# Kernel tuning notes

Measured on AMD Instinct MI355X. Metric: run time of the kernel, lower is better.

The kernel has to match this reference:

```python
import jax, jax.numpy as jnp
import numpy as np

NEG_SLOPE = 0.2  # PyG GATConv default negative_slope


def gat_conv(x, src, dst, W, a_src, a_dst, b, concat):
    """One GATConv layer (PyG semantics, self-loops already included in src/dst).

    x: [N, F_in]; src, dst: [E] int; W: [F_in, H*C]; a_src, a_dst: [H, C]; b: bias.
    """
    N = x.shape[0]
    H, C = a_src.shape
    h = (x @ W).reshape(N, H, C)                      # projected node features
    alpha_src = jnp.sum(h * a_src, axis=-1)           # [N, H]
    alpha_dst = jnp.sum(h * a_dst, axis=-1)           # [N, H]
    logits = jax.nn.leaky_relu(alpha_src[src] + alpha_dst[dst], NEG_SLOPE)  # [E, H]
    # softmax over incoming edges of each destination node (numerically stable)
    m = jax.ops.segment_max(logits, dst, num_segments=N)                    # [N, H]
    p = jnp.exp(logits - m[dst])
    denom = jax.ops.segment_sum(p, dst, num_segments=N)                     # [N, H]
    alpha = p / denom[dst]                                                  # [E, H]
    # attention-weighted scatter-add aggregation
    out = jax.ops.segment_sum(alpha[:, :, None] * h[src], dst, num_segments=N)  # [N, H, C]
    out = out.reshape(N, H * C) if concat else out.mean(axis=1)
    return out + b


def setup_inputs() -> dict:
    key = jax.random.key(0)
    ks = jax.random.split(key, 10)
    N, E = 50000, 800000
    nfeats, hidden, nclasses, in_head, out_head = 256, 32, 40, 8, 1
    s = 0.05
    return {
        "x": jax.random.normal(ks[0], (N, nfeats), dtype=jnp.float32),
        "edge_index": jax.random.randint(ks[1], (2, E), 0, N, dtype=jnp.int32),
        "w1": jax.random.normal(ks[2], (nfeats, in_head * hidden), dtype=jnp.float32) * s,
        "a_src1": jax.random.normal(ks[3], (in_head, hidden), dtype=jnp.float32) * s,
        "a_dst1": jax.random.normal(ks[4], (in_head, hidden), dtype=jnp.float32) * s,
        "b1": jnp.zeros((in_head * hidden,), dtype=jnp.float32),
        "w2": jax.random.normal(ks[5], (in_head * hidden, out_head * nclasses), dtype=jnp.float32) * s,
        "a_src2": jax.random.normal(ks[6], (out_head, nclasses), dtype=jnp.float32) * s,
        "a_dst2": jax.random.normal(ks[7], (out_head, nclasses), dtype=jnp.float32) * s,
        "b2": jnp.zeros((nclasses,), dtype=jnp.float32),
    }


def reference(x, edge_index, w1, a_src1, a_dst1, b1, w2, a_src2, a_dst2, b2):
    N = x.shape[0]
    loops = jnp.arange(N, dtype=edge_index.dtype)
    src = jnp.concatenate([edge_index[0], loops])  # PyG add_self_loops=True
    dst = jnp.concatenate([edge_index[1], loops])
    h = gat_conv(x, src, dst, w1, a_src1, a_dst1, b1, concat=True)
    h = jax.nn.elu(h)
    out = gat_conv(h, src, dst, w2, a_src2, a_dst2, b2, concat=False)
    return out
```

## Files before the change

### kernel.cpp

```cpp
#include <hip/hip_runtime.h>
#include <cstdint>
#include <cstddef>

constexpr int Nn   = 50000;
constexpr int Ee   = 800000;
constexpr int ETot = Ee + Nn;
constexpr int H1   = 8;
constexpr int C1h  = 32;
constexpr int HC1  = 256;
constexpr int C2   = 40;
constexpr int S2   = 64;
constexpr float SLOPE = 0.2f;
constexpr int NB_SCAN = (Nn + 255) / 256;

typedef __attribute__((ext_vector_type(8))) short bf16x8;
typedef __attribute__((ext_vector_type(4))) float f32x4;

__device__ __forceinline__ ushort f2bf(float f) {
    uint u = __float_as_uint(f);
    u += 0x7fffu + ((u >> 16) & 1u);
    return (ushort)(u >> 16);
}
__device__ __forceinline__ float bf2f(ushort b) {
    return __uint_as_float(((uint)b) << 16);
}

__device__ __forceinline__ void gload16(const void* g, void* lds) {
    typedef const __attribute__((address_space(1))) unsigned int GU;
    typedef __attribute__((address_space(3))) unsigned int LU;
    __builtin_amdgcn_global_load_lds((GU*)g, (LU*)lds, 16, 0, 0);
}

__global__ void k_prep(const float* __restrict__ x, ushort* __restrict__ xhi,
                       ushort* __restrict__ xlo, const float* __restrict__ w1,
                       ushort* __restrict__ WT2, const float* __restrict__ w2,
                       ushort* __restrict__ WT2b, const int* __restrict__ dstA,
                       int* __restrict__ counts) {
    int t = blockIdx.x * blockDim.x + threadIdx.x;
    constexpr int n4 = Nn * HC1 / 4;
    if (t < n4) {
        float4 v = *(const float4*)(x + (size_t)t * 4);
        ushort4 h, l;
        h.x = f2bf(v.x); l.x = f2bf(v.x - bf2f(h.x));
        h.y = f2bf(v.y); l.y = f2bf(v.y - bf2f(h.y));
        h.z = f2bf(v.z); l.z = f2bf(v.z - bf2f(h.z));
        h.w = f2bf(v.w); l.w = f2bf(v.w - bf2f(h.w));
        *(ushort4*)(xhi + (size_t)t * 4) = h;
        *(ushort4*)(xlo + (size_t)t * 4) = l;
    }
    if (t < ETot) {
        int d = (t < Ee) ? dstA[t] : t - Ee;
        atomicAdd(&counts[d], 1);
    }
    if (t < 256 * 256) {
        int k = t >> 8, col = t & 255;
        float w = w1[(size_t)k * 256 + col];
        ushort h = f2bf(w), l = f2bf(w - bf2f(h));
        int kb = k >> 3, kr = k & 7;
        WT2[((size_t)(kb)      * 256 + col) * 8 + kr] = h;
        WT2[((size_t)(kb + 32) * 256 + col) * 8 + kr] = h;
        WT2[((size_t)(kb + 64) * 256 + col) * 8 + kr] = l;
    }
    if (t < 256 * 48) {
        int k = t / 48, col = t % 48;
        float w = (col < C2) ? w2[(size_t)k * C2 + col] : 0.f;
        ushort h = f2bf(w), l = f2bf(w - bf2f(h));
        int kb = k >> 3, kr = k & 7;
        WT2b[((size_t)(kb)      * 48 + col) * 8 + kr] = h;
        WT2b[((size_t)(kb + 32) * 48 + col) * 8 + kr] = h;
        WT2b[((size_t)(kb + 64) * 48 + col) * 8 + kr] = l;
    }
}

__global__ __launch_bounds__(256) void k_scan_block(const int* __restrict__ counts,
                                                    int* __restrict__ exsc,
                                                    int* __restrict__ bsum) {
    __shared__ int sm[256];
    int i = blockIdx.x * 256 + threadIdx.x;
    int v = (i < Nn) ? counts[i] : 0;
    sm[threadIdx.x] = v;
    __syncthreads();
#pragma unroll
    for (int off = 1; off < 256; off <<= 1) {
        int t = (threadIdx.x >= off) ? sm[threadIdx.x - off] : 0;
        __syncthreads();
        sm[threadIdx.x] += t;
        __syncthreads();
    }
    if (i < Nn) exsc[i] = sm[threadIdx.x] - v;
    if (threadIdx.x == 255) bsum[blockIdx.x] = sm[255];
}

__global__ __launch_bounds__(256) void k_scan_top(const int* __restrict__ bsum,
                                                  int* __restrict__ boff) {
    __shared__ int sm[256];
    int t = threadIdx.x;
    int v = (t < NB_SCAN) ? bsum[t] : 0;
    sm[t] = v;
    __syncthreads();
#pragma unroll
    for (int off = 1; off < 256; off <<= 1) {
        int x = (t >= off) ? sm[t - off] : 0;
        __syncthreads();
        sm[t] += x;
        __syncthreads();
    }
    if (t < NB_SCAN) boff[t] = sm[t] - v;
}

__global__ void k_finalize_off(const int* __restrict__ exsc, const int* __restrict__ boff,
                               int* __restrict__ row_off, int* __restrict__ cursor) {
    int i = blockIdx.x * blockDim.x + threadIdx.x;
    if (i < Nn) {
        int r = exsc[i] + boff[i >> 8];
        row_off[i] = r;
        cursor[i] = r;
    }
    if (i == 0) row_off[Nn] = ETot;
}

__global__ void k_scatter(const int* __restrict__ srcA, const int* __restrict__ dstA,
                          int* __restrict__ cursor, int* __restrict__ csr_src) {
    int e = blockIdx.x * blockDim.x + threadIdx.x;
    if (e >= ETot) return;
    int s, d;
    if (e < Ee) { s = srcA[e]; d = dstA[e]; } else { s = e - Ee; d = s; }
    int pos = atomicAdd(&cursor[d], 1);
    csr_src[pos] = s;
}

__global__ __launch_bounds__(512, 4) void k_gemm1_mfma(const ushort* __restrict__ xhi,
                                                       const ushort* __restrict__ xlo,
                                                       const ushort* __restrict__ WT2,
                                                       ushort* __restrict__ h1b,
                                                       const float* __restrict__ a_s,
                                                       const float* __restrict__ a_d,
                                                       float* __restrict__ asrc1,
                                                       float* __restrict__ adst1, int M) {
    constexpr int BK = 32, KD = 768;
    __shared__ __align__(16) ushort As[2][128 * BK];
    __shared__ __align__(16) ushort Bs[2][256 * BK];
    const int tid = threadIdx.x;
    const int bm = blockIdx.x * 128;
    const int lane = tid & 63;
    const int wid = tid >> 6;
    const int wm = wid >> 2, wn = wid & 3;
    const int l16 = lane & 15, lk = lane >> 4;

    const int sakc = tid >> 7, sarow = tid & 127;
    int arow = bm + sarow; arow = arow < M ? arow : M - 1;

    auto stage = [&](int buf, int k0) {
        const ushort* xsec; int ks;
        if (k0 < 256)      { xsec = xhi; ks = k0; }
        else if (k0 < 512) { xsec = xlo; ks = k0 - 256; }
        else               { xsec = xhi; ks = k0 - 512; }
        gload16(xsec + (size_t)arow * 256 + ks + sakc * 8, As[buf] + tid * 8);
        const ushort* bbase = WT2 + (size_t)(k0 >> 3) * 256 * 8;
        gload16(bbase + (size_t)tid * 8,         Bs[buf] + tid * 8);
        gload16(bbase + (size_t)(512 + tid) * 8, Bs[buf] + (512 + tid) * 8);
    };

    f32x4 acc[4][4] = {};
    stage(0, 0);
    __syncthreads();
    int buf = 0;
    for (int k0 = 0; k0 < KD; k0 += BK) {
        if (k0 + BK < KD) stage(buf ^ 1, k0 + BK);
        bf16x8 a[4], b[4];
#pragma unroll
        for (int m = 0; m < 4; m++)
            a[m] = *(const bf16x8*)(As[buf] + (lk * 128 + wm * 64 + m * 16 + l16) * 8);
#pragma unroll
        for (int n = 0; n < 4; n++)
            b[n] = *(const bf16x8*)(Bs[buf] + (lk * 256 + wn * 64 + n * 16 + l16) * 8);
#pragma unroll
        for (int m = 0; m < 4; m++)
#pragma unroll
            for (int n = 0; n < 4; n++)
                acc[m][n] = __builtin_amdgcn_mfma_f32_16x16x32_bf16(a[m], b[n], acc[m][n], 0, 0, 0);
        __syncthreads();
        buf ^= 1;
    }
    float as_v[4], ad_v[4];
#pragma unroll
    for (int n = 0; n < 4; n++) {
        int col = wn * 64 + n * 16 + l16;
        as_v[n] = a_s[col];
        ad_v[n] = a_d[col];
    }
#pragma unroll
    for (int m = 0; m < 4; m++) {
#pragma unroll
        for (int j = 0; j < 4; j++) {
            int row = bm + wm * 64 + m * 16 + lk * 4 + j;
            float ps0 = acc[m][0][j] * as_v[0] + acc[m][1][j] * as_v[1];
            float ps1 = acc[m][2][j] * as_v[2] + acc[m][3][j] * as_v[3];
            float pd0 = acc[m][0][j] * ad_v[0] + acc[m][1][j] * ad_v[1];
            float pd1 = acc[m][2][j] * ad_v[2] + acc[m][3][j] * ad_v[3];
#pragma unroll
            for (int off = 1; off < 16; off <<= 1) {
                ps0 += __shfl_xor(ps0, off);
                ps1 += __shfl_xor(ps1, off);
                pd0 += __shfl_xor(pd0, off);
                pd1 += __shfl_xor(pd1, off);
            }
            if (row < M) {
#pragma unroll
                for (int n = 0; n < 4; n++)
                    h1b[(size_t)row * 256 + wn * 64 + n * 16 + l16] = f2bf(acc[m][n][j]);
                if (l16 == 0) {
                    asrc1[(size_t)row * H1 + wn * 2]     = ps0;
                    asrc1[(size_t)row * H1 + wn * 2 + 1] = ps1;
                    adst1[(size_t)row * H1 + wn * 2]     = pd0;
                    adst1[(size_t)row * H1 + wn * 2 + 1] = pd1;
                }
            }
        }
    }
}

__global__ __launch_bounds__(256, 4) void k_gemm2_mfma(const ushort* __restrict__ hi,
                                                       const ushort* __restrict__ lo,
                                                       const ushort* __restrict__ WT,
                                                       ushort* __restrict__ h2,
                                                       const float* __restrict__ a_s,
                                                       const float* __restrict__ a_d,
                                                       float* __restrict__ asrc2,
                                                       float* __restrict__ adst2, int M) {
    constexpr int BK = 32, KD = 768;
    __shared__ __align__(16) ushort As[2][128 * BK];
    __shared__ __align__(16) ushort Bs[2][48 * BK];
    const int tid = threadIdx.x;
    const int bm = blockIdx.x * 128;
    const int lane = tid & 63;
    const int w = tid >> 6;
    const int l16 = lane & 15, lk = lane >> 4;

    const int srow = tid & 127, skc = tid >> 7;
    int arow = bm + srow; arow = arow < M ? arow : M - 1;

    auto stage = [&](int buf, int k0) {
        const ushort* xsec; int ks;
        if (k0 < 256)      { xsec = hi; ks = k0; }
        else if (k0 < 512) { xsec = lo; ks = k0 - 256; }
        else               { xsec = hi; ks = k0 - 512; }
        const ushort* a_base = xsec + (size_t)arow * 256 + ks;
        gload16(a_base + skc * 8,       As[buf] + tid * 8);
        gload16(a_base + (skc + 2) * 8, As[buf] + (256 + tid) * 8);
        if (tid < 192)
            gload16(WT + ((size_t)(k0 >> 3) * 48 + tid) * 8, Bs[buf] + tid * 8);
    };

    f32x4 acc[2][3] = {};
    stage(0, 0);
    __syncthreads();
    int buf = 0;
    for (int k0 = 0; k0 < KD; k0 += BK) {
        if (k0 + BK < KD) stage(buf ^ 1, k0 + BK);
        bf16x8 a2[2], b2[3];
#pragma unroll
        for (int m = 0; m < 2; m++)
            a2[m] = *(const bf16x8*)(As[buf] + (lk * 128 + w * 32 + m * 16 + l16) * 8);
#pragma unroll
        for (int n = 0; n < 3; n++)
            b2[n] = *(const bf16x8*)(Bs[buf] + (lk * 48 + n * 16 + l16) * 8);
#pragma unroll
        for (int m = 0; m < 2; m++)
#pragma unroll
            for (int n = 0; n < 3; n++)
                acc[m][n] = __builtin_amdgcn_mfma_f32_16x16x32_bf16(a2[m], b2[n], acc[m][n], 0, 0, 0);
        __syncthreads();
        buf ^= 1;
    }
    float asv[3], adv[3];
#pragma unroll
    for (int n = 0; n < 3; n++) {
        int col = n * 16 + l16;
        asv[n] = (col < C2) ? a_s[col] : 0.f;
        adv[n] = (col < C2) ? a_d[col] : 0.f;
    }
#pragma unroll
    for (int m = 0; m < 2; m++) {
#pragma unroll
        for (int j = 0; j < 4; j++) {
            int row = bm + w * 32 + m * 16 + lk * 4 + j;
            float ps = acc[m][0][j] * asv[0] + acc[m][1][j] * asv[1] + acc[m][2][j] * asv[2];
            float pd = acc[m][0][j] * adv[0] + acc[m][1][j] * adv[1] + acc[m][2][j] * adv[2];
#pragma unroll
            for (int off = 1; off < 16; off <<= 1) {
                ps += __shfl_xor(ps, off);
                pd += __shfl_xor(pd, off);
            }
            if (row < M) {
#pragma unroll
                for (int n = 0; n < 3; n++)
                    h2[(size_t)row * S2 + n * 16 + l16] = f2bf(acc[m][n][j]);
                if (l16 == 0) { asrc2[row] = ps; adst2[row] = pd; }
            }
        }
    }
}

__global__ __launch_bounds__(256) void k_gat_aggr1(const int* __restrict__ row_off,
                                                   const int* __restrict__ csr_src,
                                                   const float* __restrict__ asrc,
                                                   const float* __restrict__ adst,
                                                   const ushort* __restrict__ h1b,
                                                   const float* __restrict__ bias,
                                                   ushort* __restrict__ o_hi,
                                                   ushort* __restrict__ o_lo) {
    int wid = (blockIdx.x * 256 + threadIdx.x) >> 6;
    if (wid >= Nn) return;
    int lane = threadIdx.x & 63;
    int half = lane >> 5, l32 = lane & 31;
    int head = l32 >> 2;
    int c0 = l32 * 8;
    int beg = row_off[wid], end = row_off[wid + 1];
    float ad = adst[(size_t)wid * H1 + head];
    float acc[8] = {};
    float sump = 0.f;
    int i = beg + half;
    for (; i + 6 < end; i += 8) {
        int s0 = csr_src[i],     s1 = csr_src[i + 2];
        int s2 = csr_src[i + 4], s3 = csr_src[i + 6];
        float a0 = asrc[(size_t)s0 * H1 + head], a1 = asrc[(size_t)s1 * H1 + head];
        float a2 = asrc[(size_t)s2 * H1 + head], a3 = asrc[(size_t)s3 * H1 + head];
        bf16x8 v0 = *(const bf16x8*)(h1b + (size_t)s0 * HC1 + c0);
        bf16x8 v1 = *(const bf16x8*)(h1b + (size_t)s1 * HC1 + c0);
        bf16x8 v2 = *(const bf16x8*)(h1b + (size_t)s2 * HC1 + c0);
        bf16x8 v3 = *(const bf16x8*)(h1b + (size_t)s3 * HC1 + c0);
        float l0 = a0 + ad; l0 = l0 > 0.f ? l0 : SLOPE * l0;
        float l1 = a1 + ad; l1 = l1 > 0.f ? l1 : SLOPE * l1;
        float l2 = a2 + ad; l2 = l2 > 0.f ? l2 : SLOPE * l2;
        float l3 = a3 + ad; l3 = l3 > 0.f ? l3 : SLOPE * l3;
        float p0 = __expf(l0), p1 = __expf(l1), p2 = __expf(l2), p3 = __expf(l3);
        sump += (p0 + p1) + (p2 + p3);
#pragma unroll
        for (int j = 0; j < 8; j++)
            acc[j] += (p0 * bf2f((ushort)v0[j]) + p1 * bf2f((ushort)v1[j])) +
                      (p2 * bf2f((ushort)v2[j]) + p3 * bf2f((ushort)v3[j]));
    }
    for (; i < end; i += 2) {
        int s = csr_src[i];
        float a = asrc[(size_t)s * H1 + head];
        bf16x8 v = *(const bf16x8*)(h1b + (size_t)s * HC1 + c0);
        float l = a + ad; l = l > 0.f ? l : SLOPE * l;
        float p = __expf(l);
        sump += p;
#pragma unroll
        for (int j = 0; j < 8; j++) acc[j] += p * bf2f((ushort)v[j]);
    }
    sump += __shfl_xor(sump, 32);
#pragma unroll
    for (int j = 0; j < 8; j++) acc[j] += __shfl_xor(acc[j], 32);
    if (half) return;
    float inv = 1.f / sump;
    float4 b0 = *(const float4*)(bias + c0);
    float4 b1 = *(const float4*)(bias + c0 + 4);
    float bb[8] = {b0.x, b0.y, b0.z, b0.w, b1.x, b1.y, b1.z, b1.w};
    uint4 uh, ul;
    uint* uhp = (uint*)&uh; uint* ulp = (uint*)&ul;
#pragma unroll
    for (int q = 0; q < 4; q++) {
        float r0 = acc[2 * q] * inv + bb[2 * q];
        float r1 = acc[2 * q + 1] * inv + bb[2 * q + 1];
        r0 = r0 > 0.f ? r0 : __expf(r0) - 1.f;
        r1 = r1 > 0.f ? r1 : __expf(r1) - 1.f;
        ushort h0 = f2bf(r0), h1v = f2bf(r1);
        ushort l0 = f2bf(r0 - bf2f(h0)), l1v = f2bf(r1 - bf2f(h1v));
        uhp[q] = (uint)h0 | ((uint)h1v << 16);
        ulp[q] = (uint)l0 | ((uint)l1v << 16);
    }
    *(uint4*)(o_hi + (size_t)wid * HC1 + c0) = uh;
    *(uint4*)(o_lo + (size_t)wid * HC1 + c0) = ul;
}

__global__ __launch_bounds__(256) void k_gat_aggr2(const int* __restrict__ row_off,
                                                   const int* __restrict__ csr_src,
                                                   const float* __restrict__ asrc,
                                                   const float* __restrict__ adst,
                                                   const ushort* __restrict__ h2,
                                                   const float* __restrict__ bias,
                                                   float* __restrict__ out) {
    int wid = (blockIdx.x * 256 + threadIdx.x) >> 6;
    if (wid >= Nn) return;
    int lane = threadIdx.x & 63;
    int cl = lane < C2 ? lane : C2 - 1;
    int beg = row_off[wid], end = row_off[wid + 1];
    float ad = adst[wid];
    float acc = 0.f, sump = 0.f;
    int i = beg;
    for (; i + 3 < end; i += 4) {
        int s0 = csr_src[i], s1 = csr_src[i + 1], s2 = csr_src[i + 2], s3 = csr_src[i + 3];
        float a0 = asrc[s0], a1 = asrc[s1], a2 = asrc[s2], a3 = asrc[s3];
        float v0 = bf2f(h2[(size_t)s0 * S2 + cl]);
        float v1 = bf2f(h2[(size_t)s1 * S2 + cl]);
        float v2 = bf2f(h2[(size_t)s2 * S2 + cl]);
        float v3 = bf2f(h2[(size_t)s3 * S2 + cl]);
        float l0 = a0 + ad; l0 = l0 > 0.f ? l0 : SLOPE * l0;
        float l1 = a1 + ad; l1 = l1 > 0.f ? l1 : SLOPE * l1;
        float l2 = a2 + ad; l2 = l2 > 0.f ? l2 : SLOPE * l2;
        float l3 = a3 + ad; l3 = l3 > 0.f ? l3 : SLOPE * l3;
        float p0 = __expf(l0), p1 = __expf(l1), p2 = __expf(l2), p3 = __expf(l3);
        sump += (p0 + p1) + (p2 + p3);
        acc += p0 * v0 + p1 * v1 + p2 * v2 + p3 * v3;
    }
    for (; i < end; i++) {
        int s = csr_src[i];
        float l = asrc[s] + ad;
        l = l > 0.f ? l : SLOPE * l;
        float pe = __expf(l);
        sump += pe;
        acc += pe * bf2f(h2[(size_t)s * S2 + cl]);
    }
    if (lane < C2) out[(size_t)wid * C2 + lane] = acc / sump + bias[lane];
}

extern "C" void kernel_launch(void* const* d_in, const int* in_sizes, int n_in,
                              void* d_out, int out_size, void* d_ws, size_t ws_size,
                              hipStream_t stream) {
    const float* x   = (const float*)d_in[0];
    const int*   ei  = (const int*)d_in[1];
    const float* w1  = (const float*)d_in[2];
    const float* as1 = (const float*)d_in[3];
    const float* ad1 = (const float*)d_in[4];
    const float* b1  = (const float*)d_in[5];
    const float* w2  = (const float*)d_in[6];
    const float* as2 = (const float*)d_in[7];
    const float* ad2 = (const float*)d_in[8];
    const float* b2  = (const float*)d_in[9];
    float* outp = (float*)d_out;

    const int* srcA = ei;
    const int* dstA = ei + Ee;

    char* W = (char*)d_ws;
    size_t o = 0;
    auto allocB = [&](size_t bytes) { void* p = W + o; o += (bytes + 255) & ~(size_t)255; return p; };

    ushort* xhi   = (ushort*)allocB((size_t)Nn * HC1 * 2);
    ushort* xlo   = (ushort*)allocB((size_t)Nn * HC1 * 2);
    ushort* o1hi  = xhi;
    ushort* o1lo  = xlo;
    ushort* wt2   = (ushort*)allocB((size_t)768 * 256 * 2);
    ushort* wt2b  = (ushort*)allocB((size_t)768 * 48 * 2);
    ushort* h1b   = (ushort*)allocB((size_t)Nn * HC1 * 2);
    ushort* h2    = (ushort*)allocB((size_t)Nn * S2 * 2);
    float*  asrc1 = (float*)allocB((size_t)Nn * H1 * 4);
    float*  adst1 = (float*)allocB((size_t)Nn * H1 * 4);
    float*  asrc2 = (float*)allocB((size_t)Nn * 4);
    float*  adst2 = (float*)allocB((size_t)Nn * 4);
    int* counts   = (int*)allocB((size_t)Nn * 4);
    int* exsc     = (int*)allocB((size_t)Nn * 4);
    int* bsum     = (int*)allocB(256 * 4);
    int* boff     = (int*)allocB(256 * 4);
    int* row_off  = (int*)allocB((size_t)(Nn + 1) * 4);
    int* cursor   = (int*)allocB((size_t)Nn * 4);
    int* csr_src  = (int*)allocB((size_t)ETot * 4);

    hipMemsetAsync(counts, 0, (size_t)Nn * sizeof(int), stream);
    k_prep<<<(Nn * HC1 / 4 + 255) / 256, 256, 0, stream>>>(
        x, xhi, xlo, w1, wt2, w2, wt2b, dstA, counts);

    k_scan_block<<<NB_SCAN, 256, 0, stream>>>(counts, exsc, bsum);
    k_scan_top<<<1, 256, 0, stream>>>(bsum, boff);
    k_finalize_off<<<(Nn + 255) / 256, 256, 0, stream>>>(exsc, boff, row_off, cursor);
    k_scatter<<<(ETot + 255) / 256, 256, 0, stream>>>(srcA, dstA, cursor, csr_src);

    k_gemm1_mfma<<<(Nn + 127) / 128, 512, 0, stream>>>(
        xhi, xlo, wt2, h1b, as1, ad1, asrc1, adst1, Nn);
    k_gat_aggr1<<<(int)(((size_t)Nn * 64 + 255) / 256), 256, 0, stream>>>(
        row_off, csr_src, asrc1, adst1, h1b, b1, o1hi, o1lo);

    k_gemm2_mfma<<<(Nn + 127) / 128, 256, 0, stream>>>(
        o1hi, o1lo, wt2b, h2, as2, ad2, asrc2, adst2, Nn);
    k_gat_aggr2<<<(int)(((size_t)Nn * 64 + 255) / 256), 256, 0, stream>>>(
        row_off, csr_src, asrc2, adst2, h2, b2, outp);
}
```

Before: 286.5 us.

## Shrink GEMM row tiles to 64 and fuse scan-top into offset finalize

The two GEMM kernels now use 64-row tiles instead of 128. GEMM1 drops to 256 threads, with each wave covering all 64 rows and one 64-column slice; GEMM2 gives each wave one 16-row MFMA tile. The aim is more blocks across the CUs (about 782 instead of 391), at the cost of reloading the weight tile more often per row. The single-block top scan and the separate finalize kernel are merged into one kernel, where every block redoes the small prefix over the block sums, which removes one launch.

```diff
diff --git a/kernel.cpp b/kernel.cpp
--- a/kernel.cpp
+++ b/kernel.cpp
@@ -91,8 +91,10 @@
     if (threadIdx.x == 255) bsum[blockIdx.x] = sm[255];
 }
 
-__global__ __launch_bounds__(256) void k_scan_top(const int* __restrict__ bsum,
-                                                  int* __restrict__ boff) {
+__global__ __launch_bounds__(256) void k_finalize2(const int* __restrict__ exsc,
+                                                   const int* __restrict__ bsum,
+                                                   int* __restrict__ row_off,
+                                                   int* __restrict__ cursor) {
     __shared__ int sm[256];
     int t = threadIdx.x;
     int v = (t < NB_SCAN) ? bsum[t] : 0;
@@ -105,14 +107,9 @@
         sm[t] += x;
         __syncthreads();
     }
-    if (t < NB_SCAN) boff[t] = sm[t] - v;
-}
-
-__global__ void k_finalize_off(const int* __restrict__ exsc, const int* __restrict__ boff,
-                               int* __restrict__ row_off, int* __restrict__ cursor) {
-    int i = blockIdx.x * blockDim.x + threadIdx.x;
+    int i = blockIdx.x * 256 + t;
     if (i < Nn) {
-        int r = exsc[i] + boff[i >> 8];
+        int r = exsc[i] + sm[blockIdx.x] - bsum[blockIdx.x];
         row_off[i] = r;
         cursor[i] = r;
     }
@@ -129,7 +126,7 @@
     csr_src[pos] = s;
 }
 
-__global__ __launch_bounds__(512, 4) void k_gemm1_mfma(const ushort* __restrict__ xhi,
+__global__ __launch_bounds__(256, 4) void k_gemm1_mfma(const ushort* __restrict__ xhi,
                                                        const ushort* __restrict__ xlo,
                                                        const ushort* __restrict__ WT2,
                                                        ushort* __restrict__ h1b,
@@ -138,16 +135,15 @@
                                                        float* __restrict__ asrc1,
                                                        float* __restrict__ adst1, int M) {
     constexpr int BK = 32, KD = 768;
-    __shared__ __align__(16) ushort As[2][128 * BK];
+    __shared__ __align__(16) ushort As[2][64 * BK];
     __shared__ __align__(16) ushort Bs[2][256 * BK];
     const int tid = threadIdx.x;
-    const int bm = blockIdx.x * 128;
+    const int bm = blockIdx.x * 64;
     const int lane = tid & 63;
-    const int wid = tid >> 6;
-    const int wm = wid >> 2, wn = wid & 3;
+    const int w = tid >> 6;
     const int l16 = lane & 15, lk = lane >> 4;
 
-    const int sakc = tid >> 7, sarow = tid & 127;
+    const int sakc = tid >> 6, sarow = tid & 63;
     int arow = bm + sarow; arow = arow < M ? arow : M - 1;
 
     auto stage = [&](int buf, int k0) {
@@ -157,8 +153,9 @@
         else               { xsec = xhi; ks = k0 - 512; }
         gload16(xsec + (size_t)arow * 256 + ks + sakc * 8, As[buf] + tid * 8);
         const ushort* bbase = WT2 + (size_t)(k0 >> 3) * 256 * 8;
-        gload16(bbase + (size_t)tid * 8,         Bs[buf] + tid * 8);
-        gload16(bbase + (size_t)(512 + tid) * 8, Bs[buf] + (512 + tid) * 8);
+#pragma unroll
+        for (int q = 0; q < 4; q++)
+            gload16(bbase + (size_t)(q * 256 + tid) * 8, Bs[buf] + (q * 256 + tid) * 8);
     };
 
     f32x4 acc[4][4] = {};
@@ -170,10 +167,10 @@
         bf16x8 a[4], b[4];
 #pragma unroll
         for (int m = 0; m < 4; m++)
-            a[m] = *(const bf16x8*)(As[buf] + (lk * 128 + wm * 64 + m * 16 + l16) * 8);
+            a[m] = *(const bf16x8*)(As[buf] + (lk * 64 + m * 16 + l16) * 8);
 #pragma unroll
         for (int n = 0; n < 4; n++)
-            b[n] = *(const bf16x8*)(Bs[buf] + (lk * 256 + wn * 64 + n * 16 + l16) * 8);
+            b[n] = *(const bf16x8*)(Bs[buf] + (lk * 256 + w * 64 + n * 16 + l16) * 8);
 #pragma unroll
         for (int m = 0; m < 4; m++)
 #pragma unroll
@@ -185,7 +182,7 @@
     float as_v[4], ad_v[4];
 #pragma unroll
     for (int n = 0; n < 4; n++) {
-        int col = wn * 64 + n * 16 + l16;
+        int col = w * 64 + n * 16 + l16;
         as_v[n] = a_s[col];
         ad_v[n] = a_d[col];
     }
@@ -193,7 +190,7 @@
     for (int m = 0; m < 4; m++) {
 #pragma unroll
         for (int j = 0; j < 4; j++) {
-            int row = bm + wm * 64 + m * 16 + lk * 4 + j;
+            int row = bm + m * 16 + lk * 4 + j;
             float ps0 = acc[m][0][j] * as_v[0] + acc[m][1][j] * as_v[1];
             float ps1 = acc[m][2][j] * as_v[2] + acc[m][3][j] * as_v[3];
             float pd0 = acc[m][0][j] * ad_v[0] + acc[m][1][j] * ad_v[1];
@@ -208,12 +205,12 @@
             if (row < M) {
 #pragma unroll
                 for (int n = 0; n < 4; n++)
-                    h1b[(size_t)row * 256 + wn * 64 + n * 16 + l16] = f2bf(acc[m][n][j]);
+                    h1b[(size_t)row * 256 + w * 64 + n * 16 + l16] = f2bf(acc[m][n][j]);
                 if (l16 == 0) {
-                    asrc1[(size_t)row * H1 + wn * 2]     = ps0;
-                    asrc1[(size_t)row * H1 + wn * 2 + 1] = ps1;
-                    adst1[(size_t)row * H1 + wn * 2]     = pd0;
-                    adst1[(size_t)row * H1 + wn * 2 + 1] = pd1;
+                    asrc1[(size_t)row * H1 + w * 2]     = ps0;
+                    asrc1[(size_t)row * H1 + w * 2 + 1] = ps1;
+                    adst1[(size_t)row * H1 + w * 2]     = pd0;
+                    adst1[(size_t)row * H1 + w * 2 + 1] = pd1;
                 }
             }
         }
@@ -229,47 +226,41 @@
                                                        float* __restrict__ asrc2,
                                                        float* __restrict__ adst2, int M) {
     constexpr int BK = 32, KD = 768;
-    __shared__ __align__(16) ushort As[2][128 * BK];
+    __shared__ __align__(16) ushort As[2][64 * BK];
     __shared__ __align__(16) ushort Bs[2][48 * BK];
     const int tid = threadIdx.x;
-    const int bm = blockIdx.x * 128;
+    const int bm = blockIdx.x * 64;
     const int lane = tid & 63;
     const int w = tid >> 6;
     const int l16 = lane & 15, lk = lane >> 4;
 
-    const int srow = tid & 127, skc = tid >> 7;
-    int arow = bm + srow; arow = arow < M ? arow : M - 1;
+    const int sakc = tid >> 6, sarow = tid & 63;
+    int arow = bm + sarow; arow = arow < M ? arow : M - 1;
 
     auto stage = [&](int buf, int k0) {
         const ushort* xsec; int ks;
         if (k0 < 256)      { xsec = hi; ks = k0; }
         else if (k0 < 512) { xsec = lo; ks = k0 - 256; }
         else               { xsec = hi; ks = k0 - 512; }
-        const ushort* a_base = xsec + (size_t)arow * 256 + ks;
-        gload16(a_base + skc * 8,       As[buf] + tid * 8);
-        gload16(a_base + (skc + 2) * 8, As[buf] + (256 + tid) * 8);
+        gload16(xsec + (size_t)arow * 256 + ks + sakc * 8, As[buf] + tid * 8);
         if (tid < 192)
             gload16(WT + ((size_t)(k0 >> 3) * 48 + tid) * 8, Bs[buf] + tid * 8);
     };
 
-    f32x4 acc[2][3] = {};
+    f32x4 acc[3] = {};
     stage(0, 0);
     __syncthreads();
     int buf = 0;
     for (int k0 = 0; k0 < KD; k0 += BK) {
         if (k0 + BK < KD) stage(buf ^ 1, k0 + BK);
-        bf16x8 a2[2], b2[3];
-#pragma unroll
-        for (int m = 0; m < 2; m++)
-            a2[m] = *(const bf16x8*)(As[buf] + (lk * 128 + w * 32 + m * 16 + l16) * 8);
+        bf16x8 a2, b2[3];
+        a2 = *(const bf16x8*)(As[buf] + (lk * 64 + w * 16 + l16) * 8);
 #pragma unroll
         for (int n = 0; n < 3; n++)
             b2[n] = *(const bf16x8*)(Bs[buf] + (lk * 48 + n * 16 + l16) * 8);
 #pragma unroll
-        for (int m = 0; m < 2; m++)
-#pragma unroll
-            for (int n = 0; n < 3; n++)
-                acc[m][n] = __builtin_amdgcn_mfma_f32_16x16x32_bf16(a2[m], b2[n], acc[m][n], 0, 0, 0);
+        for (int n = 0; n < 3; n++)
+            acc[n] = __builtin_amdgcn_mfma_f32_16x16x32_bf16(a2, b2[n], acc[n], 0, 0, 0);
         __syncthreads();
         buf ^= 1;
     }
@@ -281,23 +272,20 @@
         adv[n] = (col < C2) ? a_d[col] : 0.f;
     }
 #pragma unroll
-    for (int m = 0; m < 2; m++) {
-#pragma unroll
-        for (int j = 0; j < 4; j++) {
-            int row = bm + w * 32 + m * 16 + lk * 4 + j;
-            float ps = acc[m][0][j] * asv[0] + acc[m][1][j] * asv[1] + acc[m][2][j] * asv[2];
-            float pd = acc[m][0][j] * adv[0] + acc[m][1][j] * adv[1] + acc[m][2][j] * adv[2];
-#pragma unroll
-            for (int off = 1; off < 16; off <<= 1) {
-                ps += __shfl_xor(ps, off);
-                pd += __shfl_xor(pd, off);
-            }
-            if (row < M) {
-#pragma unroll
-                for (int n = 0; n < 3; n++)
-                    h2[(size_t)row * S2 + n * 16 + l16] = f2bf(acc[m][n][j]);
-                if (l16 == 0) { asrc2[row] = ps; adst2[row] = pd; }
-            }
+    for (int j = 0; j < 4; j++) {
+        int row = bm + w * 16 + lk * 4 + j;
+        float ps = acc[0][j] * asv[0] + acc[1][j] * asv[1] + acc[2][j] * asv[2];
+        float pd = acc[0][j] * adv[0] + acc[1][j] * adv[1] + acc[2][j] * adv[2];
+#pragma unroll
+        for (int off = 1; off < 16; off <<= 1) {
+            ps += __shfl_xor(ps, off);
+            pd += __shfl_xor(pd, off);
+        }
+        if (row < M) {
+#pragma unroll
+            for (int n = 0; n < 3; n++)
+                h2[(size_t)row * S2 + n * 16 + l16] = f2bf(acc[n][j]);
+            if (l16 == 0) { asrc2[row] = ps; adst2[row] = pd; }
         }
     }
 }
@@ -454,7 +442,6 @@
     int* counts   = (int*)allocB((size_t)Nn * 4);
     int* exsc     = (int*)allocB((size_t)Nn * 4);
     int* bsum     = (int*)allocB(256 * 4);
-    int* boff     = (int*)allocB(256 * 4);
     int* row_off  = (int*)allocB((size_t)(Nn + 1) * 4);
     int* cursor   = (int*)allocB((size_t)Nn * 4);
     int* csr_src  = (int*)allocB((size_t)ETot * 4);
@@ -464,16 +451,15 @@
         x, xhi, xlo, w1, wt2, w2, wt2b, dstA, counts);
 
     k_scan_block<<<NB_SCAN, 256, 0, stream>>>(counts, exsc, bsum);
-    k_scan_top<<<1, 256, 0, stream>>>(bsum, boff);
-    k_finalize_off<<<(Nn + 255) / 256, 256, 0, stream>>>(exsc, boff, row_off, cursor);
+    k_finalize2<<<NB_SCAN, 256, 0, stream>>>(exsc, bsum, row_off, cursor);
     k_scatter<<<(ETot + 255) / 256, 256, 0, stream>>>(srcA, dstA, cursor, csr_src);
 
-    k_gemm1_mfma<<<(Nn + 127) / 128, 512, 0, stream>>>(
+    k_gemm1_mfma<<<(Nn + 63) / 64, 256, 0, stream>>>(
         xhi, xlo, wt2, h1b, as1, ad1, asrc1, adst1, Nn);
     k_gat_aggr1<<<(int)(((size_t)Nn * 64 + 255) / 256), 256, 0, stream>>>(
         row_off, csr_src, asrc1, adst1, h1b, b1, o1hi, o1lo);
 
-    k_gemm2_mfma<<<(Nn + 127) / 128, 256, 0, stream>>>(
+    k_gemm2_mfma<<<(Nn + 63) / 64, 256, 0, stream>>>(
         o1hi, o1lo, wt2b, h2, as2, ad2, asrc2, adst2, Nn);
     k_gat_aggr2<<<(int)(((size_t)Nn * 64 + 255) / 256), 256, 0, stream>>>(
         row_off, csr_src, asrc2, adst2, h2, b2, outp);
```

Result: no change. 285.2 us (-0.5%).
